# Performance work log

Hardware: AMD Instinct MI355X
Metric: run time of the kernel (lower is better)

## Reference

```python
import jax, jax.numpy as jnp
import numpy as np


def setup_inputs() -> dict:
    key = jax.random.key(0)
    ks = jax.random.split(key, 4)
    C, CK = 256, 32  # in_channels, in_channels // 8
    B, H, W = 16, 64, 64
    x = jax.random.normal(ks[0], (B, C, H, W), dtype=jnp.float32)
    # conv1x1 weights (kernel spatial dims squeezed), scaled like kaiming-ish init
    Wq = jax.random.normal(ks[1], (CK, C), dtype=jnp.float32) / np.sqrt(C)
    Wk = jax.random.normal(ks[2], (CK, C), dtype=jnp.float32) / np.sqrt(C)
    Wv = jax.random.normal(ks[3], (C, C), dtype=jnp.float32) / np.sqrt(C)
    bq = jnp.zeros((CK,), jnp.float32)
    bk = jnp.zeros((CK,), jnp.float32)
    bv = jnp.zeros((C,), jnp.float32)
    alpha = jnp.zeros((1,), jnp.float32)  # nn.Parameter(torch.zeros(1))
    return {"x": x, "Wq": Wq, "bq": bq, "Wk": Wk, "bk": bk,
            "Wv": Wv, "bv": bv, "alpha": alpha}


def reference(x, Wq, bq, Wk, bk, Wv, bv, alpha):
    B, C, H, W = x.shape
    N = H * W
    xf = x.reshape(B, C, N)  # [B, C, N]
    # 1x1 convs == per-pixel linear projections
    q = jnp.einsum('oc,bcn->bno', Wq, xf) + bq          # [B, N, CK]  (query, permuted)
    k = jnp.einsum('oc,bcn->bon', Wk, xf) + bk[:, None]  # [B, CK, N]
    v = jnp.einsum('oc,bcn->bon', Wv, xf) + bv[:, None]  # [B, C, N]
    # NOTE: faithful to source -- no 1/sqrt(d) scaling
    scores = jnp.einsum('bno,bom->bnm', q, k)            # [B, N, N]
    attn = jax.nn.softmax(scores, axis=-1)               # softmax over keys
    # out = value @ attention^T : out[:, :, i] = sum_j attn[i, j] * v[:, :, j]
    out = jnp.einsum('bcm,bnm->bcn', v, attn).reshape(B, C, H, W)
    return alpha[0] * out + x
```

## Files before the change

kernel.cpp:

```cpp
#include <hip/hip_runtime.h>
#include <cstdint>
#include <cstddef>

#define BN 16
#define CC 256
#define CKD 32
#define NN 4096

typedef __attribute__((ext_vector_type(8))) short s8v;
typedef __attribute__((ext_vector_type(4))) float f4v;
typedef __attribute__((ext_vector_type(4))) unsigned int u4v;
typedef __attribute__((ext_vector_type(2))) unsigned int u2v;
typedef unsigned short ushort_t;

#define L2E 1.44269504088896340736f

__device__ __forceinline__ ushort_t f2bf(float f) {
    union { float f; uint32_t u; } v; v.f = f;
    uint32_t u = v.u + 0x7FFFu + ((v.u >> 16) & 1u);
    return (ushort_t)(u >> 16);
}
__device__ __forceinline__ uint32_t fbits(float f) {
    union { float f; uint32_t u; } v; v.f = f; return v.u;
}
__device__ __forceinline__ float exp2_hw(float x) {
    float r; asm("v_exp_f32 %0, %1" : "=v"(r) : "v"(x)); return r;
}
__device__ __forceinline__ uint32_t pkbf(float lo, float hi) {
    return __builtin_amdgcn_perm(fbits(hi), fbits(lo), 0x07060302u);
}
__device__ __forceinline__ uint32_t pkbf_rne(float lo, float hi) {
    return (uint32_t)f2bf(lo) | ((uint32_t)f2bf(hi) << 16);
}

__global__ __launch_bounds__(256) void proj_all(
    const float* __restrict__ x,
    const float* __restrict__ Wq, const float* __restrict__ bq,
    const float* __restrict__ Wk, const float* __restrict__ bk,
    const float* __restrict__ Wv, const float* __restrict__ bv,
    ushort_t* __restrict__ qw, ushort_t* __restrict__ kw, ushort_t* __restrict__ vw)
{
    __shared__ __align__(16) ushort_t As[64 * 264];

    int b  = blockIdx.y;
    int n0 = blockIdx.x * 64;
    int tid = threadIdx.x;
    int wave = tid >> 6, lane = tid & 63;
    int lq = lane & 15, quad = lane >> 4;
    int n = n0 + wave * 16 + lq;

    const float* xb = x + (size_t)b * CC * NN + n;
    s8v bb[8];
#pragma unroll
    for (int h = 0; h < 8; h++) {
        const float* src = xb + (size_t)(h * 32 + quad * 8) * NN;
        float t0 = src[0 * NN];
        float t1 = src[1 * NN];
        float t2 = src[2 * NN];
        float t3 = src[3 * NN];
        float t4 = src[4 * NN];
        float t5 = src[5 * NN];
        float t6 = src[6 * NN];
        float t7 = src[7 * NN];
        s8v p;
        p[0] = (short)f2bf(t0); p[1] = (short)f2bf(t1);
        p[2] = (short)f2bf(t2); p[3] = (short)f2bf(t3);
        p[4] = (short)f2bf(t4); p[5] = (short)f2bf(t5);
        p[6] = (short)f2bf(t6); p[7] = (short)f2bf(t7);
        bb[h] = p;
    }

    int arow = tid >> 2;
    int kseg = (tid & 3) * 64;

    for (int mten = 0; mten < 5; mten++) {
        int m0 = mten * 64;
        __syncthreads();

        {
            int am = m0 + arow;
            const float* wrow;
            if (am < 32)       wrow = Wq + (size_t)am * CC;
            else if (am < 64)  wrow = Wk + (size_t)(am - 32) * CC;
            else               wrow = Wv + (size_t)(am - 64) * CC;
#pragma unroll
            for (int g = 0; g < 8; g++) {
                f4v f0 = *reinterpret_cast<const f4v*>(wrow + kseg + g * 8);
                f4v f1 = *reinterpret_cast<const f4v*>(wrow + kseg + g * 8 + 4);
                s8v p;
                p[0] = (short)f2bf(f0[0]); p[1] = (short)f2bf(f0[1]);
                p[2] = (short)f2bf(f0[2]); p[3] = (short)f2bf(f0[3]);
                p[4] = (short)f2bf(f1[0]); p[5] = (short)f2bf(f1[1]);
                p[6] = (short)f2bf(f1[2]); p[7] = (short)f2bf(f1[3]);
                *reinterpret_cast<s8v*>(&As[arow * 264 + kseg + g * 8]) = p;
            }
        }
        __syncthreads();

        f4v acc[4];
#pragma unroll
        for (int i = 0; i < 4; i++) acc[i] = (f4v){0.f, 0.f, 0.f, 0.f};
#pragma unroll
        for (int h = 0; h < 8; h++) {
            s8v a[4];
#pragma unroll
            for (int mt = 0; mt < 4; mt++)
                a[mt] = *reinterpret_cast<const s8v*>(
                    &As[(mt * 16 + lq) * 264 + h * 32 + quad * 8]);
#pragma unroll
            for (int mt = 0; mt < 4; mt++)
                acc[mt] = __builtin_amdgcn_mfma_f32_16x16x32_bf16(
                    a[mt], bb[h], acc[mt], 0, 0, 0);
        }

        if (mten == 0) {
#pragma unroll
            for (int mt = 0; mt < 2; mt++) {
                int ck = mt * 16 + quad * 4;
                float v0 = (acc[mt][0] + bq[ck + 0]) * L2E;
                float v1 = (acc[mt][1] + bq[ck + 1]) * L2E;
                float v2 = (acc[mt][2] + bq[ck + 2]) * L2E;
                float v3 = (acc[mt][3] + bq[ck + 3]) * L2E;
                u2v w;
                w[0] = pkbf_rne(v0, v1);
                w[1] = pkbf_rne(v2, v3);
                *reinterpret_cast<u2v*>(qw + ((size_t)b * NN + n) * CKD + ck) = w;
            }
#pragma unroll
            for (int mt = 0; mt < 2; mt++) {
                int ck = mt * 16 + quad * 4;
                float v0 = acc[mt + 2][0] + bk[ck + 0];
                float v1 = acc[mt + 2][1] + bk[ck + 1];
                float v2 = acc[mt + 2][2] + bk[ck + 2];
                float v3 = acc[mt + 2][3] + bk[ck + 3];
                u2v w;
                w[0] = pkbf_rne(v0, v1);
                w[1] = pkbf_rne(v2, v3);
                *reinterpret_cast<u2v*>(kw + ((size_t)b * NN + n) * CKD + ck) = w;
            }
        } else {
#pragma unroll
            for (int mt = 0; mt < 4; mt++)
#pragma unroll
                for (int r = 0; r < 4; r++) {
                    int c = (m0 - 64) + mt * 16 + quad * 4 + r;
                    vw[((size_t)b * CC + c) * NN + n] = f2bf(acc[mt][r] + bv[c]);
                }
        }
    }
}

__global__ __launch_bounds__(512, 4) void attn(
    const ushort_t* __restrict__ qw, const ushort_t* __restrict__ kw,
    const ushort_t* __restrict__ vw, const float* __restrict__ x,
    const float* __restrict__ alpha, float* __restrict__ out)
{
    __shared__ __align__(16) ushort_t Pl[2][128 * 72];
    __shared__ __align__(16) ushort_t Kl[2][64 * 32];
    __shared__ float lL[128];

    int b = blockIdx.y;
    int q0 = blockIdx.x * 128;
    int tid = threadIdx.x;
    int wq = tid >> 6, lane = tid & 63;
    int lq = lane & 15, quad = lane >> 4;

    const ushort_t* kbase = kw + (size_t)b * NN * CKD;
    const ushort_t* vbase = vw + (size_t)b * CC * NN;

    int krow = tid >> 3;
    int kcol = (tid & 7) * 4;
    const ushort_t* ksrc = kbase + (size_t)krow * CKD + kcol;

    int kro[4];
#pragma unroll
    for (int nt = 0; nt < 4; nt++)
        kro[nt] = (32 * (nt >> 1) + 2 * (lq & 12) + 4 * (nt & 1) + (lq & 3)) * 32 + quad * 8;

    const ushort_t* vrow0 = vbase + (size_t)(wq * 32 + lq) * NN;
    const ushort_t* vrow1 = vbase + (size_t)(wq * 32 + 16 + lq) * NN;

    const s8v qf = *reinterpret_cast<const s8v*>(
        qw + ((size_t)b * NN + q0 + wq * 16 + lq) * CKD + quad * 8);

    f4v acc[8][2];
#pragma unroll
    for (int i = 0; i < 8; i++) {
        acc[i][0] = (f4v){0.f, 0.f, 0.f, 0.f};
        acc[i][1] = (f4v){0.f, 0.f, 0.f, 0.f};
    }
    float srow = 0.f;

    u2v k0 = *reinterpret_cast<const u2v*>(ksrc);
    u2v k1 = *reinterpret_cast<const u2v*>(ksrc + (size_t)64 * CKD);
    u2v kst = *reinterpret_cast<const u2v*>(ksrc + (size_t)128 * CKD);
    s8v v00 = *reinterpret_cast<const s8v*>(vrow0 + quad * 8);
    s8v v01 = *reinterpret_cast<const s8v*>(vrow0 + 32 + quad * 8);
    s8v v10 = *reinterpret_cast<const s8v*>(vrow1 + quad * 8);
    s8v v11 = *reinterpret_cast<const s8v*>(vrow1 + 32 + quad * 8);
    *reinterpret_cast<u2v*>(&Kl[0][krow * 32 + kcol]) = k0;
    *reinterpret_cast<u2v*>(&Kl[1][krow * 32 + kcol]) = k1;
    __syncthreads();

    for (int kt = 0; kt < 64; kt++) {
        const int cur = kt & 1;

        s8v pa0, pa1;
        {
            s8v kf0 = *reinterpret_cast<const s8v*>(&Kl[cur][kro[0]]);
            s8v kf1 = *reinterpret_cast<const s8v*>(&Kl[cur][kro[1]]);
            f4v sA = __builtin_amdgcn_mfma_f32_16x16x32_bf16(kf0, qf, (f4v){0.f,0.f,0.f,0.f}, 0, 0, 0);
            f4v sB = __builtin_amdgcn_mfma_f32_16x16x32_bf16(kf1, qf, (f4v){0.f,0.f,0.f,0.f}, 0, 0, 0);
            s8v kf2 = *reinterpret_cast<const s8v*>(&Kl[cur][kro[2]]);
            s8v kf3 = *reinterpret_cast<const s8v*>(&Kl[cur][kro[3]]);
            f4v sC = __builtin_amdgcn_mfma_f32_16x16x32_bf16(kf2, qf, (f4v){0.f,0.f,0.f,0.f}, 0, 0, 0);
            f4v sD = __builtin_amdgcn_mfma_f32_16x16x32_bf16(kf3, qf, (f4v){0.f,0.f,0.f,0.f}, 0, 0, 0);
            float a0 = exp2_hw(sA[0]), a1 = exp2_hw(sA[1]), a2 = exp2_hw(sA[2]), a3 = exp2_hw(sA[3]);
            float b0 = exp2_hw(sB[0]), b1 = exp2_hw(sB[1]), b2 = exp2_hw(sB[2]), b3 = exp2_hw(sB[3]);
            srow += ((a0 + a1) + (a2 + a3)) + ((b0 + b1) + (b2 + b3));
            union { u4v u; s8v s; } t0;
            t0.u[0] = pkbf(a0, a1); t0.u[1] = pkbf(a2, a3);
            t0.u[2] = pkbf(b0, b1); t0.u[3] = pkbf(b2, b3);
            pa0 = t0.s;
            float c0 = exp2_hw(sC[0]), c1 = exp2_hw(sC[1]), c2 = exp2_hw(sC[2]), c3 = exp2_hw(sC[3]);
            float d0 = exp2_hw(sD[0]), d1 = exp2_hw(sD[1]), d2 = exp2_hw(sD[2]), d3 = exp2_hw(sD[3]);
            srow += ((c0 + c1) + (c2 + c3)) + ((d0 + d1) + (d2 + d3));
            union { u4v u; s8v s; } t1;
            t1.u[0] = pkbf(c0, c1); t1.u[1] = pkbf(c2, c3);
            t1.u[2] = pkbf(d0, d1); t1.u[3] = pkbf(d2, d3);
            pa1 = t1.s;
        }

        {
            int prow = (wq * 16 + lq) * 72;
            *reinterpret_cast<s8v*>(&Pl[cur][prow + quad * 8]) = pa0;
            *reinterpret_cast<s8v*>(&Pl[cur][prow + 32 + quad * 8]) = pa1;
        }

        __syncthreads();
        __builtin_amdgcn_sched_barrier(0);

        *reinterpret_cast<u2v*>(&Kl[cur][krow * 32 + kcol]) = kst;

        __builtin_amdgcn_s_setprio(1);
#pragma unroll
        for (int qt = 0; qt < 8; qt++) {
            s8v pA0 = *reinterpret_cast<const s8v*>(&Pl[cur][(qt * 16 + lq) * 72 + quad * 8]);
            s8v pA1 = *reinterpret_cast<const s8v*>(&Pl[cur][(qt * 16 + lq) * 72 + 32 + quad * 8]);
            acc[qt][0] = __builtin_amdgcn_mfma_f32_16x16x32_bf16(pA0, v00, acc[qt][0], 0, 0, 0);
            acc[qt][0] = __builtin_amdgcn_mfma_f32_16x16x32_bf16(pA1, v01, acc[qt][0], 0, 0, 0);
            acc[qt][1] = __builtin_amdgcn_mfma_f32_16x16x32_bf16(pA0, v10, acc[qt][1], 0, 0, 0);
            acc[qt][1] = __builtin_amdgcn_mfma_f32_16x16x32_bf16(pA1, v11, acc[qt][1], 0, 0, 0);
        }
        __builtin_amdgcn_s_setprio(0);

        {
            int kbn = (kt + 1 < 64 ? kt + 1 : 63) * 64;
            v00 = *reinterpret_cast<const s8v*>(vrow0 + kbn + quad * 8);
            v01 = *reinterpret_cast<const s8v*>(vrow0 + kbn + 32 + quad * 8);
            v10 = *reinterpret_cast<const s8v*>(vrow1 + kbn + quad * 8);
            v11 = *reinterpret_cast<const s8v*>(vrow1 + kbn + 32 + quad * 8);
            int kn = (kt + 3 < 64 ? kt + 3 : 63) * 64;
            kst = *reinterpret_cast<const u2v*>(ksrc + (size_t)kn * CKD);
        }
    }

    srow += __shfl_xor(srow, 16, 64);
    srow += __shfl_xor(srow, 32, 64);
    if (quad == 0) lL[wq * 16 + lq] = srow;
    __syncthreads();

    float a0 = alpha[0];
#pragma unroll
    for (int qt = 0; qt < 8; qt++) {
        float li[4];
#pragma unroll
        for (int r = 0; r < 4; r++) li[r] = 1.0f / lL[qt * 16 + quad * 4 + r];
#pragma unroll
        for (int ct = 0; ct < 2; ct++) {
            int c = wq * 32 + ct * 16 + lq;
            size_t idx = ((size_t)b * CC + c) * NN + q0 + qt * 16 + quad * 4;
            f4v xv = *reinterpret_cast<const f4v*>(x + idx);
            f4v o;
#pragma unroll
            for (int r = 0; r < 4; r++) o[r] = a0 * (acc[qt][ct][r] * li[r]) + xv[r];
            *reinterpret_cast<f4v*>(out + idx) = o;
        }
    }
}

extern "C" void kernel_launch(void* const* d_in, const int* in_sizes, int n_in,
                              void* d_out, int out_size, void* d_ws, size_t ws_size,
                              hipStream_t stream) {
    (void)in_sizes; (void)n_in; (void)out_size; (void)ws_size;
    const float* x     = (const float*)d_in[0];
    const float* Wq    = (const float*)d_in[1];
    const float* bq    = (const float*)d_in[2];
    const float* Wk    = (const float*)d_in[3];
    const float* bk    = (const float*)d_in[4];
    const float* Wv    = (const float*)d_in[5];
    const float* bv    = (const float*)d_in[6];
    const float* alpha = (const float*)d_in[7];
    float* out = (float*)d_out;

    char* ws = (char*)d_ws;
    ushort_t* qw = (ushort_t*)ws;
    ushort_t* kw = (ushort_t*)(ws + (size_t)BN * NN * CKD * 2);
    ushort_t* vw = (ushort_t*)(ws + (size_t)2 * BN * NN * CKD * 2);

    proj_all<<<dim3(64, BN), 256, 0, stream>>>(x, Wq, bq, Wk, bk, Wv, bv, qw, kw, vw);
    attn    <<<dim3(NN / 128, BN), 512, 0, stream>>>(qw, kw, vw, x, alpha, out);
}
```

Baseline: 318.8 us.

## Pre-convert projection weights to bf16 once and read them directly from global

A new small kernel converts Wq/Wk/Wv to one packed bf16 buffer, stored temporarily in the output buffer. The projection kernel then drops its per-block fp32 weight load, conversion, LDS staging and barriers, and reads weight fragments straight from global/L2. It also issues all 64 x loads up front to raise memory-level parallelism. This adds a kernel launch and depends on the attention kernel fully overwriting the output, and uncached global reads replace LDS reads.

New measurement: 340.0 us. 1.07x slower.

```diff
diff --git a/kernel.cpp b/kernel.cpp
--- a/kernel.cpp
+++ b/kernel.cpp
@@ -33,15 +33,29 @@
     return (uint32_t)f2bf(lo) | ((uint32_t)f2bf(hi) << 16);
 }
 
+__global__ __launch_bounds__(256) void wconv(
+    const float* __restrict__ Wq, const float* __restrict__ Wk,
+    const float* __restrict__ Wv, ushort_t* __restrict__ wbf)
+{
+    int e = (blockIdx.x * 256 + threadIdx.x) * 4;
+    int m = e >> 8, k = e & 255;
+    const float* src;
+    if (m < 32)       src = Wq + (size_t)m * CC + k;
+    else if (m < 64)  src = Wk + (size_t)(m - 32) * CC + k;
+    else              src = Wv + (size_t)(m - 64) * CC + k;
+    f4v f = *reinterpret_cast<const f4v*>(src);
+    u2v w;
+    w[0] = pkbf_rne(f[0], f[1]);
+    w[1] = pkbf_rne(f[2], f[3]);
+    *reinterpret_cast<u2v*>(wbf + e) = w;
+}
+
 __global__ __launch_bounds__(256) void proj_all(
-    const float* __restrict__ x,
-    const float* __restrict__ Wq, const float* __restrict__ bq,
-    const float* __restrict__ Wk, const float* __restrict__ bk,
-    const float* __restrict__ Wv, const float* __restrict__ bv,
+    const float* __restrict__ x, const ushort_t* __restrict__ wbf,
+    const float* __restrict__ bq, const float* __restrict__ bk,
+    const float* __restrict__ bv,
     ushort_t* __restrict__ qw, ushort_t* __restrict__ kw, ushort_t* __restrict__ vw)
 {
-    __shared__ __align__(16) ushort_t As[64 * 264];
-
     int b  = blockIdx.y;
     int n0 = blockIdx.x * 64;
     int tid = threadIdx.x;
@@ -50,53 +64,25 @@
     int n = n0 + wave * 16 + lq;
 
     const float* xb = x + (size_t)b * CC * NN + n;
+    float xr[64];
+#pragma unroll
+    for (int h = 0; h < 8; h++)
+#pragma unroll
+        for (int j = 0; j < 8; j++)
+            xr[h * 8 + j] = xb[(size_t)(h * 32 + quad * 8 + j) * NN];
     s8v bb[8];
 #pragma unroll
     for (int h = 0; h < 8; h++) {
-        const float* src = xb + (size_t)(h * 32 + quad * 8) * NN;
-        float t0 = src[0 * NN];
-        float t1 = src[1 * NN];
-        float t2 = src[2 * NN];
-        float t3 = src[3 * NN];
-        float t4 = src[4 * NN];
-        float t5 = src[5 * NN];
-        float t6 = src[6 * NN];
-        float t7 = src[7 * NN];
         s8v p;
-        p[0] = (short)f2bf(t0); p[1] = (short)f2bf(t1);
-        p[2] = (short)f2bf(t2); p[3] = (short)f2bf(t3);
-        p[4] = (short)f2bf(t4); p[5] = (short)f2bf(t5);
-        p[6] = (short)f2bf(t6); p[7] = (short)f2bf(t7);
+#pragma unroll
+        for (int j = 0; j < 8; j++) p[j] = (short)f2bf(xr[h * 8 + j]);
         bb[h] = p;
     }
 
-    int arow = tid >> 2;
-    int kseg = (tid & 3) * 64;
-
+    const ushort_t* wb = wbf + lq * 256 + quad * 8;
+
+#pragma unroll
     for (int mten = 0; mten < 5; mten++) {
-        int m0 = mten * 64;
-        __syncthreads();
-
-        {
-            int am = m0 + arow;
-            const float* wrow;
-            if (am < 32)       wrow = Wq + (size_t)am * CC;
-            else if (am < 64)  wrow = Wk + (size_t)(am - 32) * CC;
-            else               wrow = Wv + (size_t)(am - 64) * CC;
-#pragma unroll
-            for (int g = 0; g < 8; g++) {
-                f4v f0 = *reinterpret_cast<const f4v*>(wrow + kseg + g * 8);
-                f4v f1 = *reinterpret_cast<const f4v*>(wrow + kseg + g * 8 + 4);
-                s8v p;
-                p[0] = (short)f2bf(f0[0]); p[1] = (short)f2bf(f0[1]);
-                p[2] = (short)f2bf(f0[2]); p[3] = (short)f2bf(f0[3]);
-                p[4] = (short)f2bf(f1[0]); p[5] = (short)f2bf(f1[1]);
-                p[6] = (short)f2bf(f1[2]); p[7] = (short)f2bf(f1[3]);
-                *reinterpret_cast<s8v*>(&As[arow * 264 + kseg + g * 8]) = p;
-            }
-        }
-        __syncthreads();
-
         f4v acc[4];
 #pragma unroll
         for (int i = 0; i < 4; i++) acc[i] = (f4v){0.f, 0.f, 0.f, 0.f};
@@ -106,7 +92,7 @@
 #pragma unroll
             for (int mt = 0; mt < 4; mt++)
                 a[mt] = *reinterpret_cast<const s8v*>(
-                    &As[(mt * 16 + lq) * 264 + h * 32 + quad * 8]);
+                    wb + (mten * 64 + mt * 16) * 256 + h * 32);
 #pragma unroll
             for (int mt = 0; mt < 4; mt++)
                 acc[mt] = __builtin_amdgcn_mfma_f32_16x16x32_bf16(
@@ -143,7 +129,7 @@
             for (int mt = 0; mt < 4; mt++)
 #pragma unroll
                 for (int r = 0; r < 4; r++) {
-                    int c = (m0 - 64) + mt * 16 + quad * 4 + r;
+                    int c = (mten - 1) * 64 + mt * 16 + quad * 4 + r;
                     vw[((size_t)b * CC + c) * NN + n] = f2bf(acc[mt][r] + bv[c]);
                 }
         }
@@ -307,7 +293,9 @@
     ushort_t* qw = (ushort_t*)ws;
     ushort_t* kw = (ushort_t*)(ws + (size_t)BN * NN * CKD * 2);
     ushort_t* vw = (ushort_t*)(ws + (size_t)2 * BN * NN * CKD * 2);
-
-    proj_all<<<dim3(64, BN), 256, 0, stream>>>(x, Wq, bq, Wk, bk, Wv, bv, qw, kw, vw);
+    ushort_t* wbf = (ushort_t*)d_out;
+
+    wconv   <<<dim3(80), 256, 0, stream>>>(Wq, Wk, Wv, wbf);
+    proj_all<<<dim3(64, BN), 256, 0, stream>>>(x, wbf, bq, bk, bv, qw, kw, vw);
     attn    <<<dim3(NN / 128, BN), 512, 0, stream>>>(qw, kw, vw, x, alpha, out);
 }
```
